# Kernel optimization log

Measured on AMD Instinct MI355X. Metric: run time of the kernel, lower is better.

The kernel has to match this reference:

```python
import jax, jax.numpy as jnp
import numpy as np

N = 50000   # nodes (= batch_size = num_e)
D = 256     # d_dim = n_hidden
E = 320000  # edges (first half 'in' direction, second half 'out'/inverse)
R = 400     # relation types (incl. inverses)


def setup_inputs() -> dict:
    key = jax.random.key(0)
    ks = jax.random.split(key, 12)
    s = 0.05  # weight scale so tanh stays in linear-ish range
    w = lambda k, shp: jax.random.normal(k, shp, jnp.float32) * s
    return {
        "emb": jax.random.normal(ks[0], (N, D), jnp.float32),
        "edge_index": jax.random.randint(ks[1], (2, E), 0, N),
        "edge_type": jax.random.randint(ks[2], (E,), 0, R),
        "rel1": w(ks[3], (R, D)),
        "W_in1": w(ks[4], (D, D)),
        "W_out1": w(ks[5], (D, D)),
        "W_loop1": w(ks[6], (D, D)),
        "b1": jnp.zeros((D,), jnp.float32),
        "rel2": w(ks[7], (R, D)),
        "W_in2": w(ks[8], (D, D)),
        "W_out2": w(ks[9], (D, D)),
        "W_loop2": w(ks[10], (D, D)),
        "b2": jnp.zeros((D,), jnp.float32),
        "res": jnp.array([0.1], jnp.float32),
        "mu_w": w(ks[11], (D, D)),
        "mu_b": jnp.zeros((D,), jnp.float32),
        "num_nodes": N,
    }


def _mgcn_conv(x, edge_index, edge_type, rel, W_in, W_out, W_loop, b, n):
    """Relational conv: gather -> compose with relation emb -> direction-split
    linear transform -> degree-normalized scatter-add -> self-loop -> tanh."""
    src, dst = edge_index[0], edge_index[1]
    e = edge_index.shape[1]
    half = e // 2
    m = x[src] * rel[edge_type]                                   # [E, D] compose ('mult')
    m = jnp.concatenate([m[:half] @ W_in, m[half:] @ W_out], 0)    # direction-specific transform
    deg = jax.ops.segment_sum(jnp.ones((e,), x.dtype), dst, num_segments=n)
    norm = 1.0 / jnp.maximum(deg, 1.0)                             # 1/in-degree
    agg = jax.ops.segment_sum(m * norm[dst][:, None], dst, num_segments=n)
    return jnp.tanh(agg + x @ W_loop + b)


def reference(emb, edge_index, edge_type,
              rel1, W_in1, W_out1, W_loop1, b1,
              rel2, W_in2, W_out2, W_loop2, b2,
              res, mu_w, mu_b, num_nodes):
    # forward_base with p.res=True, core_layer=2, dropout in eval mode (identity)
    h = emb + res * _mgcn_conv(emb, edge_index, edge_type, rel1, W_in1, W_out1, W_loop1, b1, num_nodes)
    h = h + res * _mgcn_conv(h, edge_index, edge_type, rel2, W_in2, W_out2, W_loop2, b2, num_nodes)
    # drift head f(t, y) = mu(forward_base(y))
    return h @ mu_w + mu_b
```

## Files before the change

### kernel.cpp

```cpp
#include <hip/hip_runtime.h>
#include <hip/hip_bf16.h>
#include <cstdint>
#include <cstddef>


typedef short bf16x8 __attribute__((ext_vector_type(8)));
typedef float f32x4  __attribute__((ext_vector_type(4)));

__device__ __forceinline__ float b2f(unsigned short u) {
    union { unsigned u32; float f; } c; c.u32 = ((unsigned)u) << 16; return c.f;
}
__device__ __forceinline__ unsigned short f2b(float f) {
    union { float f; unsigned u; } c; c.f = f;
    unsigned r = c.u + 0x7FFFu + ((c.u >> 16) & 1u);
    return (unsigned short)(r >> 16);
}
__device__ __forceinline__ float ftanh(float x) {
    float e = __expf(2.0f * x);
    return 1.0f - __fdividef(2.0f, e + 1.0f);
}


__global__ void k_hist(const int* __restrict__ dst, int* __restrict__ cnt, int E) {
    int i = blockIdx.x * blockDim.x + threadIdx.x;
    if (i < E) atomicAdd(&cnt[dst[i]], 1);
}

__global__ void k_norm(const int* __restrict__ cnt, float* __restrict__ norm, int N) {
    int i = blockIdx.x * blockDim.x + threadIdx.x;
    if (i < N) norm[i] = 1.0f / fmaxf((float)cnt[i], 1.0f);
}

__global__ void k_scan1(const int* __restrict__ cnt, int* __restrict__ part,
                        int* __restrict__ bsum, int N) {
    __shared__ int s[256];
    int i = blockIdx.x * 256 + threadIdx.x;
    int v = (i < N) ? cnt[i] : 0;
    s[threadIdx.x] = v; __syncthreads();
    #pragma unroll
    for (int o = 1; o < 256; o <<= 1) {
        int t = (threadIdx.x >= o) ? s[threadIdx.x - o] : 0;
        __syncthreads();
        s[threadIdx.x] += t;
        __syncthreads();
    }
    if (i < N) part[i] = s[threadIdx.x] - v;
    if (threadIdx.x == 255) bsum[blockIdx.x] = s[255];
}

__global__ void k_scan2(int* __restrict__ bsum, int nb) {
    __shared__ int s[256];
    int v = (threadIdx.x < nb) ? bsum[threadIdx.x] : 0;
    s[threadIdx.x] = v; __syncthreads();
    #pragma unroll
    for (int o = 1; o < 256; o <<= 1) {
        int t = (threadIdx.x >= o) ? s[threadIdx.x - o] : 0;
        __syncthreads();
        s[threadIdx.x] += t;
        __syncthreads();
    }
    if (threadIdx.x < nb) bsum[threadIdx.x] = s[threadIdx.x] - v;
}

__global__ void k_scan3(const int* __restrict__ part, const int* __restrict__ bsum,
                        int* __restrict__ rowptr, int* __restrict__ cursor, int N, int E) {
    int i = blockIdx.x * 256 + threadIdx.x;
    if (i < N) {
        int r = part[i] + bsum[blockIdx.x];
        rowptr[i] = r; cursor[i] = r;
    }
    if (i == 0) rowptr[N] = E;
}

__global__ void k_scatter(const int* __restrict__ src, const int* __restrict__ dst,
                          const int* __restrict__ et, int* __restrict__ cursor,
                          unsigned* __restrict__ erec, int E, int halfE) {
    int e = blockIdx.x * blockDim.x + threadIdx.x;
    if (e < E) {
        int d = dst[e];
        int pos = atomicAdd(&cursor[d], 1);
        unsigned rec = (unsigned)src[e] | ((unsigned)et[e] << 16)
                     | ((e >= halfE) ? 0x80000000u : 0u);
        erec[pos] = rec;
    }
}


__global__ void k_cvt3(const float* __restrict__ s0, unsigned short* __restrict__ d0, long n0,
                       const float* __restrict__ s1, unsigned short* __restrict__ d1, long n1,
                       const float* __restrict__ s2, unsigned short* __restrict__ d2, long n2) {
    long i = (long)blockIdx.x * blockDim.x + threadIdx.x;
    const float* s; unsigned short* d; long j = i;
    if (j < n0) { s = s0; d = d0; }
    else {
        j -= n0;
        if (j < n1) { s = s1; d = d1; }
        else { j -= n1; if (j >= n2) return; s = s2; d = d2; }
    }
    float4 v = ((const float4*)s)[j];
    ushort4 o;
    o.x = f2b(v.x); o.y = f2b(v.y); o.z = f2b(v.z); o.w = f2b(v.w);
    ((ushort4*)d)[j] = o;
}

__global__ void k_wfrag7(const float* __restrict__ w0, const float* __restrict__ w1,
                         const float* __restrict__ w2, const float* __restrict__ w3,
                         const float* __restrict__ w4, const float* __restrict__ w5,
                         const float* __restrict__ w6, unsigned short* __restrict__ out) {
    int o = blockIdx.x * 256 + threadIdx.x;
    int mi = o >> 16;
    int r  = o & 65535;
    const float* W = (mi == 0) ? w0 : (mi == 1) ? w1 : (mi == 2) ? w2 :
                     (mi == 3) ? w3 : (mi == 4) ? w4 : (mi == 5) ? w5 : w6;
    int j  = r & 7;
    int l  = (r >> 3) & 63;
    int nn = (r >> 9) & 15;
    int kg = r >> 13;
    int k = kg * 32 + (l >> 4) * 8 + j;
    int n = nn * 16 + (l & 15);
    out[o] = f2b(W[k * 256 + n]);
}


__global__ __launch_bounds__(256)
void k_agg(const unsigned short* __restrict__ xb, const unsigned short* __restrict__ relb,
           const int* __restrict__ rowptr, const unsigned* __restrict__ erec,
           const float* __restrict__ norm,
           unsigned short* __restrict__ sIn, unsigned short* __restrict__ sOut,
           int N, int D)
{
    const int w = threadIdx.x >> 6, l = threadIdx.x & 63;
    const int v = blockIdx.x * 4 + w;
    if (v >= N) return;
    const int rs = rowptr[v], re = rowptr[v + 1];
    const float nm = norm[v];

    float ai0 = 0, ai1 = 0, ai2 = 0, ai3 = 0;
    float ao0 = 0, ao1 = 0, ao2 = 0, ao3 = 0;

    unsigned c0 = (rs     < re) ? erec[rs]     : 0u;
    unsigned c1 = (rs + 1 < re) ? erec[rs + 1] : 0u;
    unsigned c2 = (rs + 2 < re) ? erec[rs + 2] : 0u;
    unsigned c3 = (rs + 3 < re) ? erec[rs + 3] : 0u;
    int i = rs;
    while (i + 4 <= re) {
        unsigned m0 = (i + 4 < re) ? erec[i + 4] : 0u;
        unsigned m1 = (i + 5 < re) ? erec[i + 5] : 0u;
        unsigned m2 = (i + 6 < re) ? erec[i + 6] : 0u;
        unsigned m3 = (i + 7 < re) ? erec[i + 7] : 0u;
        ushort4 x0 = *(const ushort4*)(xb   + (size_t)(c0 & 0xffff) * D + l * 4);
        ushort4 r0 = *(const ushort4*)(relb + (size_t)((c0 >> 16) & 0x7fff) * D + l * 4);
        ushort4 x1 = *(const ushort4*)(xb   + (size_t)(c1 & 0xffff) * D + l * 4);
        ushort4 r1 = *(const ushort4*)(relb + (size_t)((c1 >> 16) & 0x7fff) * D + l * 4);
        ushort4 x2 = *(const ushort4*)(xb   + (size_t)(c2 & 0xffff) * D + l * 4);
        ushort4 r2 = *(const ushort4*)(relb + (size_t)((c2 >> 16) & 0x7fff) * D + l * 4);
        ushort4 x3 = *(const ushort4*)(xb   + (size_t)(c3 & 0xffff) * D + l * 4);
        ushort4 r3 = *(const ushort4*)(relb + (size_t)((c3 >> 16) & 0x7fff) * D + l * 4);
        float p0, p1, p2, p3;
        p0 = b2f(x0.x)*b2f(r0.x); p1 = b2f(x0.y)*b2f(r0.y);
        p2 = b2f(x0.z)*b2f(r0.z); p3 = b2f(x0.w)*b2f(r0.w);
        if (c0 >> 31) { ao0 += p0; ao1 += p1; ao2 += p2; ao3 += p3; }
        else          { ai0 += p0; ai1 += p1; ai2 += p2; ai3 += p3; }
        p0 = b2f(x1.x)*b2f(r1.x); p1 = b2f(x1.y)*b2f(r1.y);
        p2 = b2f(x1.z)*b2f(r1.z); p3 = b2f(x1.w)*b2f(r1.w);
        if (c1 >> 31) { ao0 += p0; ao1 += p1; ao2 += p2; ao3 += p3; }
        else          { ai0 += p0; ai1 += p1; ai2 += p2; ai3 += p3; }
        p0 = b2f(x2.x)*b2f(r2.x); p1 = b2f(x2.y)*b2f(r2.y);
        p2 = b2f(x2.z)*b2f(r2.z); p3 = b2f(x2.w)*b2f(r2.w);
        if (c2 >> 31) { ao0 += p0; ao1 += p1; ao2 += p2; ao3 += p3; }
        else          { ai0 += p0; ai1 += p1; ai2 += p2; ai3 += p3; }
        p0 = b2f(x3.x)*b2f(r3.x); p1 = b2f(x3.y)*b2f(r3.y);
        p2 = b2f(x3.z)*b2f(r3.z); p3 = b2f(x3.w)*b2f(r3.w);
        if (c3 >> 31) { ao0 += p0; ao1 += p1; ao2 += p2; ao3 += p3; }
        else          { ai0 += p0; ai1 += p1; ai2 += p2; ai3 += p3; }
        c0 = m0; c1 = m1; c2 = m2; c3 = m3; i += 4;
    }
    #pragma unroll
    for (int j = 0; j < 3; ++j) {
        if (i + j < re) {
            unsigned cur = (j == 0) ? c0 : (j == 1) ? c1 : c2;
            ushort4 x0 = *(const ushort4*)(xb   + (size_t)(cur & 0xffff) * D + l * 4);
            ushort4 r0 = *(const ushort4*)(relb + (size_t)((cur >> 16) & 0x7fff) * D + l * 4);
            float p0 = b2f(x0.x)*b2f(r0.x), p1 = b2f(x0.y)*b2f(r0.y);
            float p2 = b2f(x0.z)*b2f(r0.z), p3 = b2f(x0.w)*b2f(r0.w);
            if (cur >> 31) { ao0 += p0; ao1 += p1; ao2 += p2; ao3 += p3; }
            else           { ai0 += p0; ai1 += p1; ai2 += p2; ai3 += p3; }
        }
    }

    ushort4 oi, oo;
    oi.x = f2b(ai0 * nm); oi.y = f2b(ai1 * nm); oi.z = f2b(ai2 * nm); oi.w = f2b(ai3 * nm);
    oo.x = f2b(ao0 * nm); oo.y = f2b(ao1 * nm); oo.z = f2b(ao2 * nm); oo.w = f2b(ao3 * nm);
    *(ushort4*)(sIn  + (size_t)v * D + l * 4) = oi;
    *(ushort4*)(sOut + (size_t)v * D + l * 4) = oo;
}


#define GIT(S, AtC, AtN, Rw0, Rw1, Rl0, Rl1)                                    \
  do {                                                                          \
    if ((S) + 1 < 12) {                                                         \
      *(uint4*)(&AtN[wo0]) = Rw0;                                               \
      *(uint4*)(&AtN[wo1]) = Rw1;                                               \
    }                                                                           \
    {                                                                           \
      const int p_ = (S) >> 2, cb_ = (S) & 3;                                   \
      const unsigned short* __restrict__ Wp_ = Wf + (size_t)p_ * 65536;         \
      _Pragma("unroll")                                                         \
      for (int kk_ = 0; kk_ < 2; ++kk_) {                                       \
        const int kg_ = cb_ * 2 + kk_;                                          \
        bf16x8 a_[4], b_[4];                                                    \
        _Pragma("unroll")                                                       \
        for (int m_ = 0; m_ < 4; ++m_) {                                        \
          int rm_ = 16 * m_ + lr;                                               \
          int ch_ = (kk_ * 4 + lq) ^ (rm_ & 7);                                 \
          a_[m_] = *(const bf16x8*)(&AtC[rm_ * 64 + ch_ * 8]);                  \
        }                                                                       \
        _Pragma("unroll")                                                       \
        for (int n_ = 0; n_ < 4; ++n_) {                                        \
          b_[n_] = *(const bf16x8*)(Wp_ + (((kg_ * 16 + (w * 4 + n_)) * 64 + l) * 8)); \
        }                                                                       \
        _Pragma("unroll")                                                       \
        for (int m_ = 0; m_ < 4; ++m_) {                                        \
          _Pragma("unroll")                                                     \
          for (int n_ = 0; n_ < 4; ++n_) {                                      \
            acc[m_][n_] = __builtin_amdgcn_mfma_f32_16x16x32_bf16(a_[m_], b_[n_], acc[m_][n_], 0, 0, 0); \
          }                                                                     \
        }                                                                       \
      }                                                                         \
    }                                                                           \
    if ((S) + 3 < 12) {                                                         \
      const int p3_ = ((S) + 3) >> 2, cb3_ = ((S) + 3) & 3;                     \
      const unsigned short* ap_ = (p3_ == 0) ? a0 : ((p3_ == 1) ? a1 : a2);     \
      Rl0 = *(const uint4*)(ap_ + g0 + cb3_ * 64);                              \
      Rl1 = *(const uint4*)(ap_ + g1 + cb3_ * 64);                              \
    }                                                                           \
    asm volatile("s_waitcnt lgkmcnt(0)" ::: "memory");                          \
    __builtin_amdgcn_sched_barrier(0);                                          \
    __builtin_amdgcn_s_barrier();                                               \
    __builtin_amdgcn_sched_barrier(0);                                          \
  } while (0)

template <bool HEAD>
__global__ __launch_bounds__(256, 4)
void k_gemm(const unsigned short* __restrict__ a0,
            const unsigned short* __restrict__ a1,
            const unsigned short* __restrict__ a2,
            const unsigned short* __restrict__ Wf,
            const float* __restrict__ bias,
            const float* __restrict__ resPtr,
            const unsigned short* __restrict__ WfMu,
            const float* __restrict__ mub,
            float* __restrict__ outF,
            unsigned short* __restrict__ outB,
            int N, int D)
{
    __shared__ unsigned short lds[HEAD ? 16384 : 8192];
    unsigned short* At0 = lds;
    unsigned short* At1 = lds + 4096;

    const int t = threadIdx.x;
    const int rBase = blockIdx.x * 64;

    const int w  = t >> 6;
    const int l  = t & 63;
    const int lr = l & 15;
    const int lq = l >> 4;

    const int rS0 = t >> 3;
    const int rS1 = rS0 + 32;
    const int cS  = t & 7;
    const int wo0 = rS0 * 64 + ((cS ^ (rS0 & 7)) * 8);
    const int wo1 = rS1 * 64 + ((cS ^ (rS1 & 7)) * 8);
    const size_t g0 = (size_t)min(rBase + rS0, N - 1) * D + cS * 8;
    const size_t g1 = (size_t)min(rBase + rS1, N - 1) * D + cS * 8;

    f32x4 acc[4][4] = {};
    uint4 Ra0, Ra1, Rb0, Rb1, Rc0, Rc1;

    Ra0 = *(const uint4*)(a0 + g0);
    Ra1 = *(const uint4*)(a0 + g1);
    Rb0 = *(const uint4*)(a0 + g0 + 64);
    Rb1 = *(const uint4*)(a0 + g1 + 64);
    Rc0 = *(const uint4*)(a0 + g0 + 128);
    Rc1 = *(const uint4*)(a0 + g1 + 128);
    *(uint4*)(&At0[wo0]) = Ra0;
    *(uint4*)(&At0[wo1]) = Ra1;
    asm volatile("s_waitcnt lgkmcnt(0)" ::: "memory");
    __builtin_amdgcn_sched_barrier(0);
    __builtin_amdgcn_s_barrier();
    __builtin_amdgcn_sched_barrier(0);

    GIT(0,  At0, At1, Rb0, Rb1, Ra0, Ra1);
    GIT(1,  At1, At0, Rc0, Rc1, Rb0, Rb1);
    GIT(2,  At0, At1, Ra0, Ra1, Rc0, Rc1);
    GIT(3,  At1, At0, Rb0, Rb1, Ra0, Ra1);
    GIT(4,  At0, At1, Rc0, Rc1, Rb0, Rb1);
    GIT(5,  At1, At0, Ra0, Ra1, Rc0, Rc1);
    GIT(6,  At0, At1, Rb0, Rb1, Ra0, Ra1);
    GIT(7,  At1, At0, Rc0, Rc1, Rb0, Rb1);
    GIT(8,  At0, At1, Ra0, Ra1, Rc0, Rc1);
    GIT(9,  At1, At0, Rb0, Rb1, Ra0, Ra1);
    GIT(10, At0, At1, Rc0, Rc1, Rb0, Rb1);
    GIT(11, At1, At0, Ra0, Ra1, Rc0, Rc1);

    const int rb4 = lq * 4;
    const float resv = resPtr[0];

    if (!HEAD) {
        unsigned short* C = lds;
        #pragma unroll
        for (int half = 0; half < 2; ++half) {
            if ((w >> 1) == half) {
                #pragma unroll
                for (int m = 0; m < 4; ++m) {
                    #pragma unroll
                    for (int i = 0; i < 4; ++i) {
                        int r6 = 16 * m + rb4 + i;
                        #pragma unroll
                        for (int n = 0; n < 4; ++n) {
                            int cH = (w & 1) * 64 + lr + 16 * n;
                            float v = acc[m][n][i] + bias[half * 128 + cH];
                            C[r6 * 128 + cH] = f2b(resv * ftanh(v));
                        }
                    }
                }
            }
            __syncthreads();
            #pragma unroll
            for (int ii = 0; ii < 4; ++ii) {
                int g   = ii * 256 + t;
                int r   = g >> 4;
                int cc  = g & 15;
                int row = rBase + r;
                if (row < N) {
                    bf16x8 sv = *(const bf16x8*)(&C[r * 128 + cc * 8]);
                    const unsigned short* ar = a0 + (size_t)row * D + half * 128 + cc * 8;
                    uint4 av = *(const uint4*)ar;
                    unsigned aw[4] = { av.x, av.y, av.z, av.w };
                    unsigned ow[4];
                    #pragma unroll
                    for (int p = 0; p < 4; ++p) {
                        float h0 = b2f((unsigned short)(aw[p] & 0xffff)) + b2f((unsigned short)sv[2 * p]);
                        float h1 = b2f((unsigned short)(aw[p] >> 16))    + b2f((unsigned short)sv[2 * p + 1]);
                        ow[p] = (unsigned)f2b(h0) | ((unsigned)f2b(h1) << 16);
                    }
                    *(uint4*)(outB + (size_t)row * D + half * 128 + cc * 8) =
                        make_uint4(ow[0], ow[1], ow[2], ow[3]);
                }
            }
            __syncthreads();
        }
    } else {
        #pragma unroll
        for (int m = 0; m < 4; ++m) {
            #pragma unroll
            for (int i = 0; i < 4; ++i) {
                int row = rBase + 16 * m + rb4 + i;
                if (row < N) {
                    size_t base = (size_t)row * D + w * 64 + lr;
                    int r6 = 16 * m + rb4 + i;
                    #pragma unroll
                    for (int n = 0; n < 4; ++n) {
                        int   c = w * 64 + lr + 16 * n;
                        float v = acc[m][n][i] + bias[c];
                        float h = b2f(a0[base + 16 * n]) + resv * ftanh(v);
                        lds[r6 * 256 + (c ^ ((r6 & 7) << 3))] = f2b(h);
                    }
                }
            }
        }
        __syncthreads();
        #pragma unroll
        for (int m = 0; m < 4; ++m) {
            #pragma unroll
            for (int n = 0; n < 4; ++n)
                acc[m][n] = (f32x4){0.f, 0.f, 0.f, 0.f};
        }

        #pragma unroll
        for (int s2 = 0; s2 < 4; ++s2) {
            #pragma unroll
            for (int kk = 0; kk < 2; ++kk) {
                const int kg = s2 * 2 + kk;
                bf16x8 a_[4], b_[4];
                #pragma unroll
                for (int m = 0; m < 4; ++m) {
                    int rm = 16 * m + lr;
                    int ch = (s2 * 8 + kk * 4 + lq) ^ (rm & 7);
                    a_[m] = *(const bf16x8*)(&lds[rm * 256 + ch * 8]);
                }
                #pragma unroll
                for (int n = 0; n < 4; ++n)
                    b_[n] = *(const bf16x8*)(WfMu + (((kg * 16 + (w * 4 + n)) * 64 + l) * 8));
                #pragma unroll
                for (int m = 0; m < 4; ++m) {
                    #pragma unroll
                    for (int n = 0; n < 4; ++n)
                        acc[m][n] = __builtin_amdgcn_mfma_f32_16x16x32_bf16(a_[m], b_[n], acc[m][n], 0, 0, 0);
                }
            }
        }

        __syncthreads();
        float* Cf = (float*)lds;
        #pragma unroll
        for (int half = 0; half < 2; ++half) {
            if ((w >> 1) == half) {
                #pragma unroll
                for (int m = 0; m < 4; ++m) {
                    #pragma unroll
                    for (int i = 0; i < 4; ++i) {
                        int r6 = 16 * m + rb4 + i;
                        #pragma unroll
                        for (int n = 0; n < 4; ++n) {
                            int cH = (w & 1) * 64 + lr + 16 * n;
                            Cf[r6 * 128 + cH] = acc[m][n][i] + mub[half * 128 + cH];
                        }
                    }
                }
            }
            __syncthreads();
            #pragma unroll
            for (int ii = 0; ii < 8; ++ii) {
                int g   = ii * 256 + t;
                int r   = g >> 5;
                int cc  = g & 31;
                int row = rBase + r;
                if (row < N) {
                    *(float4*)(outF + (size_t)row * D + half * 128 + cc * 4) =
                        *(const float4*)(&Cf[r * 128 + cc * 4]);
                }
            }
            __syncthreads();
        }
    }
}


extern "C" void kernel_launch(void* const* d_in, const int* in_sizes, int n_in,
                              void* d_out, int out_size, void* d_ws, size_t ws_size,
                              hipStream_t stream)
{
    const float* emb  = (const float*)d_in[0];
    const int*   ei   = (const int*)  d_in[1];
    const int*   et   = (const int*)  d_in[2];
    const float* rel1 = (const float*)d_in[3];
    const float* Wi1  = (const float*)d_in[4];
    const float* Wo1  = (const float*)d_in[5];
    const float* Wl1  = (const float*)d_in[6];
    const float* b1   = (const float*)d_in[7];
    const float* rel2 = (const float*)d_in[8];
    const float* Wi2  = (const float*)d_in[9];
    const float* Wo2  = (const float*)d_in[10];
    const float* Wl2  = (const float*)d_in[11];
    const float* b2   = (const float*)d_in[12];
    const float* res  = (const float*)d_in[13];
    const float* muw  = (const float*)d_in[14];
    const float* mub  = (const float*)d_in[15];

    const int D = in_sizes[7];
    const int N = in_sizes[0] / D;
    const int E = in_sizes[2];
    const int R = in_sizes[3] / D;
    const int halfE = E / 2;
    const int* srcA = ei;
    const int* dstA = ei + E;
    const size_t DD = (size_t)D * D;

    char* ws = (char*)d_ws;
    size_t off = 0;
    auto alloc = [&](size_t bytes) -> char* {
        char* p = ws + off; off += (bytes + 255) & ~(size_t)255; return p;
    };
    const int nb1 = (N + 255) / 256;

    float*          norm   = (float*)          alloc((size_t)N * 4);
    int*            cnt    = (int*)            alloc((size_t)N * 4);
    int*            rowptr = (int*)            alloc((size_t)(N + 1) * 4);
    int*            cursor = (int*)            alloc((size_t)N * 4);
    int*            part   = (int*)            alloc((size_t)N * 4);
    int*            bsum   = (int*)            alloc(1024);
    unsigned*       erec   = (unsigned*)       alloc((size_t)E * 4);
    unsigned short* xb     = (unsigned short*) alloc((size_t)N * D * 2);
    unsigned short* h1b    = (unsigned short*) alloc((size_t)N * D * 2);
    unsigned short* sIn    = (unsigned short*) alloc((size_t)N * D * 2);
    unsigned short* sOut   = (unsigned short*) alloc((size_t)N * D * 2);
    unsigned short* r1b    = (unsigned short*) alloc((size_t)R * D * 2);
    unsigned short* r2b    = (unsigned short*) alloc((size_t)R * D * 2);
    unsigned short* fAll   = (unsigned short*) alloc(7 * DD * 2);
    if (off > ws_size) return;

    unsigned short* fW1 = fAll;
    unsigned short* fW2 = fAll + 3 * DD;
    unsigned short* fMu = fAll + 6 * DD;

    hipMemsetAsync(cnt, 0, (size_t)N * 4, stream);
    k_hist   <<<(E + 255) / 256, 256, 0, stream>>>(dstA, cnt, E);
    k_norm   <<<nb1, 256, 0, stream>>>(cnt, norm, N);
    k_scan1  <<<nb1, 256, 0, stream>>>(cnt, part, bsum, N);
    k_scan2  <<<1,   256, 0, stream>>>(bsum, nb1);
    k_scan3  <<<nb1, 256, 0, stream>>>(part, bsum, rowptr, cursor, N, E);
    k_scatter<<<(E + 255) / 256, 256, 0, stream>>>(srcA, dstA, et, cursor, erec, E, halfE);

    long nd4 = (long)N * D / 4, rd4 = (long)R * D / 4;
    long tot4 = nd4 + 2 * rd4;
    k_cvt3<<<(int)((tot4 + 255) / 256), 256, 0, stream>>>(
        emb, xb, nd4, rel1, r1b, rd4, rel2, r2b, rd4);
    k_wfrag7<<<(int)(7 * DD / 256), 256, 0, stream>>>(
        Wl1, Wi1, Wo1, Wl2, Wi2, Wo2, muw, fAll);

    const int AB = (N + 3) / 4;
    const int NB = (N + 63) / 64;

    k_agg<<<AB, 256, 0, stream>>>(xb, r1b, rowptr, erec, norm, sIn, sOut, N, D);
    k_gemm<false><<<NB, 256, 0, stream>>>(xb, sIn, sOut, fW1, b1, res,
                                          nullptr, nullptr, nullptr, h1b, N, D);

    k_agg<<<AB, 256, 0, stream>>>(h1b, r2b, rowptr, erec, norm, sIn, sOut, N, D);
    k_gemm<true><<<NB, 256, 0, stream>>>(h1b, sIn, sOut, fW2, b2, res,
                                         fMu, mub, (float*)d_out, nullptr, N, D);
}
```

Baseline: 240.7 us.

## Double-buffer weight fragments in registers to prefetch next k-step

The GEMM main loop now loads the next stage's weight (B) fragments from global memory into a second register buffer while the current stage's MFMAs run from the first, instead of loading B right before use. This is meant to hide global-load latency for the weights. Launch bounds drop from 4 to 2 blocks per SM so the extra 16 vector registers fit, which lowers potential occupancy.

```diff
diff --git a/kernel.cpp b/kernel.cpp
--- a/kernel.cpp
+++ b/kernel.cpp
@@ -196,19 +196,30 @@
 }
 
 
-#define GIT(S, AtC, AtN, Rw0, Rw1, Rl0, Rl1)                                    \
+#define GIT(S, AtC, AtN, Rw0, Rw1, Rl0, Rl1, Bc, Bn)                            \
   do {                                                                          \
     if ((S) + 1 < 12) {                                                         \
       *(uint4*)(&AtN[wo0]) = Rw0;                                               \
       *(uint4*)(&AtN[wo1]) = Rw1;                                               \
     }                                                                           \
-    {                                                                           \
-      const int p_ = (S) >> 2, cb_ = (S) & 3;                                   \
-      const unsigned short* __restrict__ Wp_ = Wf + (size_t)p_ * 65536;         \
+    if ((S) + 1 < 12) {                                                         \
+      const int pn_ = ((S) + 1) >> 2, cbn_ = ((S) + 1) & 3;                     \
+      const unsigned short* __restrict__ Wn_ = Wf + (size_t)pn_ * 65536;        \
       _Pragma("unroll")                                                         \
       for (int kk_ = 0; kk_ < 2; ++kk_) {                                       \
-        const int kg_ = cb_ * 2 + kk_;                                          \
-        bf16x8 a_[4], b_[4];                                                    \
+        _Pragma("unroll")                                                       \
+        for (int n_ = 0; n_ < 4; ++n_) {                                        \
+          Bn[kk_ * 4 + n_] = *(const bf16x8*)(Wn_ +                             \
+              ((((cbn_ * 2 + kk_) * 16 + (w * 4 + n_)) * 64 + l) * 8));         \
+        }                                                                       \
+      }                                                                         \
+    }                                                                           \
+    {                                                                           \
+      const int cb_ = (S) & 3;                                                  \
+      _Pragma("unroll")                                                         \
+      for (int kk_ = 0; kk_ < 2; ++kk_) {                                       \
+        (void)cb_;                                                              \
+        bf16x8 a_[4];                                                           \
         _Pragma("unroll")                                                       \
         for (int m_ = 0; m_ < 4; ++m_) {                                        \
           int rm_ = 16 * m_ + lr;                                               \
@@ -216,14 +227,10 @@
           a_[m_] = *(const bf16x8*)(&AtC[rm_ * 64 + ch_ * 8]);                  \
         }                                                                       \
         _Pragma("unroll")                                                       \
-        for (int n_ = 0; n_ < 4; ++n_) {                                        \
-          b_[n_] = *(const bf16x8*)(Wp_ + (((kg_ * 16 + (w * 4 + n_)) * 64 + l) * 8)); \
-        }                                                                       \
-        _Pragma("unroll")                                                       \
         for (int m_ = 0; m_ < 4; ++m_) {                                        \
           _Pragma("unroll")                                                     \
           for (int n_ = 0; n_ < 4; ++n_) {                                      \
-            acc[m_][n_] = __builtin_amdgcn_mfma_f32_16x16x32_bf16(a_[m_], b_[n_], acc[m_][n_], 0, 0, 0); \
+            acc[m_][n_] = __builtin_amdgcn_mfma_f32_16x16x32_bf16(a_[m_], Bc[kk_ * 4 + n_], acc[m_][n_], 0, 0, 0); \
           }                                                                     \
         }                                                                       \
       }                                                                         \
@@ -241,7 +248,7 @@
   } while (0)
 
 template <bool HEAD>
-__global__ __launch_bounds__(256, 4)
+__global__ __launch_bounds__(256, 2)
 void k_gemm(const unsigned short* __restrict__ a0,
             const unsigned short* __restrict__ a1,
             const unsigned short* __restrict__ a2,
@@ -276,6 +283,7 @@
 
     f32x4 acc[4][4] = {};
     uint4 Ra0, Ra1, Rb0, Rb1, Rc0, Rc1;
+    bf16x8 B0[8], B1[8];
 
     Ra0 = *(const uint4*)(a0 + g0);
     Ra1 = *(const uint4*)(a0 + g1);
@@ -283,6 +291,12 @@
     Rb1 = *(const uint4*)(a0 + g1 + 64);
     Rc0 = *(const uint4*)(a0 + g0 + 128);
     Rc1 = *(const uint4*)(a0 + g1 + 128);
+    #pragma unroll
+    for (int kk = 0; kk < 2; ++kk) {
+        #pragma unroll
+        for (int n = 0; n < 4; ++n)
+            B0[kk * 4 + n] = *(const bf16x8*)(Wf + (((kk * 16 + (w * 4 + n)) * 64 + l) * 8));
+    }
     *(uint4*)(&At0[wo0]) = Ra0;
     *(uint4*)(&At0[wo1]) = Ra1;
     asm volatile("s_waitcnt lgkmcnt(0)" ::: "memory");
@@ -290,18 +304,18 @@
     __builtin_amdgcn_s_barrier();
     __builtin_amdgcn_sched_barrier(0);
 
-    GIT(0,  At0, At1, Rb0, Rb1, Ra0, Ra1);
-    GIT(1,  At1, At0, Rc0, Rc1, Rb0, Rb1);
-    GIT(2,  At0, At1, Ra0, Ra1, Rc0, Rc1);
-    GIT(3,  At1, At0, Rb0, Rb1, Ra0, Ra1);
-    GIT(4,  At0, At1, Rc0, Rc1, Rb0, Rb1);
-    GIT(5,  At1, At0, Ra0, Ra1, Rc0, Rc1);
-    GIT(6,  At0, At1, Rb0, Rb1, Ra0, Ra1);
-    GIT(7,  At1, At0, Rc0, Rc1, Rb0, Rb1);
-    GIT(8,  At0, At1, Ra0, Ra1, Rc0, Rc1);
-    GIT(9,  At1, At0, Rb0, Rb1, Ra0, Ra1);
-    GIT(10, At0, At1, Rc0, Rc1, Rb0, Rb1);
-    GIT(11, At1, At0, Ra0, Ra1, Rc0, Rc1);
+    GIT(0,  At0, At1, Rb0, Rb1, Ra0, Ra1, B0, B1);
+    GIT(1,  At1, At0, Rc0, Rc1, Rb0, Rb1, B1, B0);
+    GIT(2,  At0, At1, Ra0, Ra1, Rc0, Rc1, B0, B1);
+    GIT(3,  At1, At0, Rb0, Rb1, Ra0, Ra1, B1, B0);
+    GIT(4,  At0, At1, Rc0, Rc1, Rb0, Rb1, B0, B1);
+    GIT(5,  At1, At0, Ra0, Ra1, Rc0, Rc1, B1, B0);
+    GIT(6,  At0, At1, Rb0, Rb1, Ra0, Ra1, B0, B1);
+    GIT(7,  At1, At0, Rc0, Rc1, Rb0, Rb1, B1, B0);
+    GIT(8,  At0, At1, Ra0, Ra1, Rc0, Rc1, B0, B1);
+    GIT(9,  At1, At0, Rb0, Rb1, Ra0, Ra1, B1, B0);
+    GIT(10, At0, At1, Rc0, Rc1, Rb0, Rb1, B0, B1);
+    GIT(11, At1, At0, Ra0, Ra1, Rc0, Rc1, B1, B0);
 
     const int rb4 = lq * 4;
     const float resv = resPtr[0];
```

Result: faster. 229.1 us (-4.8%).

## Load GEMM A operands directly from global memory, dropping LDS staging pipeline

Applied to the files above, without the earlier changes.

Replaces the register-prefetched, double-buffered LDS staging of the A tile (with a barrier per k-step) with direct per-lane global loads of A fragments feeding MFMA, all three input parts walked in one unrolled loop. This removes the LDS writes, the LDS reads and the twelve block barriers, but each wave now loads its own A rows from global/L2 with no software prefetch, so latency is hidden only by occupancy and the compiler's scheduling. Launch bounds drop to 3 blocks per SM to allow more registers, and the epilogue barrier is moved so the trailing sync is skipped.

```diff
diff --git a/kernel.cpp b/kernel.cpp
--- a/kernel.cpp
+++ b/kernel.cpp
@@ -196,52 +196,8 @@
 }
 
 
-#define GIT(S, AtC, AtN, Rw0, Rw1, Rl0, Rl1)                                    \
-  do {                                                                          \
-    if ((S) + 1 < 12) {                                                         \
-      *(uint4*)(&AtN[wo0]) = Rw0;                                               \
-      *(uint4*)(&AtN[wo1]) = Rw1;                                               \
-    }                                                                           \
-    {                                                                           \
-      const int p_ = (S) >> 2, cb_ = (S) & 3;                                   \
-      const unsigned short* __restrict__ Wp_ = Wf + (size_t)p_ * 65536;         \
-      _Pragma("unroll")                                                         \
-      for (int kk_ = 0; kk_ < 2; ++kk_) {                                       \
-        const int kg_ = cb_ * 2 + kk_;                                          \
-        bf16x8 a_[4], b_[4];                                                    \
-        _Pragma("unroll")                                                       \
-        for (int m_ = 0; m_ < 4; ++m_) {                                        \
-          int rm_ = 16 * m_ + lr;                                               \
-          int ch_ = (kk_ * 4 + lq) ^ (rm_ & 7);                                 \
-          a_[m_] = *(const bf16x8*)(&AtC[rm_ * 64 + ch_ * 8]);                  \
-        }                                                                       \
-        _Pragma("unroll")                                                       \
-        for (int n_ = 0; n_ < 4; ++n_) {                                        \
-          b_[n_] = *(const bf16x8*)(Wp_ + (((kg_ * 16 + (w * 4 + n_)) * 64 + l) * 8)); \
-        }                                                                       \
-        _Pragma("unroll")                                                       \
-        for (int m_ = 0; m_ < 4; ++m_) {                                        \
-          _Pragma("unroll")                                                     \
-          for (int n_ = 0; n_ < 4; ++n_) {                                      \
-            acc[m_][n_] = __builtin_amdgcn_mfma_f32_16x16x32_bf16(a_[m_], b_[n_], acc[m_][n_], 0, 0, 0); \
-          }                                                                     \
-        }                                                                       \
-      }                                                                         \
-    }                                                                           \
-    if ((S) + 3 < 12) {                                                         \
-      const int p3_ = ((S) + 3) >> 2, cb3_ = ((S) + 3) & 3;                     \
-      const unsigned short* ap_ = (p3_ == 0) ? a0 : ((p3_ == 1) ? a1 : a2);     \
-      Rl0 = *(const uint4*)(ap_ + g0 + cb3_ * 64);                              \
-      Rl1 = *(const uint4*)(ap_ + g1 + cb3_ * 64);                              \
-    }                                                                           \
-    asm volatile("s_waitcnt lgkmcnt(0)" ::: "memory");                          \
-    __builtin_amdgcn_sched_barrier(0);                                          \
-    __builtin_amdgcn_s_barrier();                                               \
-    __builtin_amdgcn_sched_barrier(0);                                          \
-  } while (0)
-
 template <bool HEAD>
-__global__ __launch_bounds__(256, 4)
+__global__ __launch_bounds__(256, 3)
 void k_gemm(const unsigned short* __restrict__ a0,
             const unsigned short* __restrict__ a1,
             const unsigned short* __restrict__ a2,
@@ -255,8 +211,6 @@
             int N, int D)
 {
     __shared__ unsigned short lds[HEAD ? 16384 : 8192];
-    unsigned short* At0 = lds;
-    unsigned short* At1 = lds + 4096;
 
     const int t = threadIdx.x;
     const int rBase = blockIdx.x * 64;
@@ -266,42 +220,36 @@
     const int lr = l & 15;
     const int lq = l >> 4;
 
-    const int rS0 = t >> 3;
-    const int rS1 = rS0 + 32;
-    const int cS  = t & 7;
-    const int wo0 = rS0 * 64 + ((cS ^ (rS0 & 7)) * 8);
-    const int wo1 = rS1 * 64 + ((cS ^ (rS1 & 7)) * 8);
-    const size_t g0 = (size_t)min(rBase + rS0, N - 1) * D + cS * 8;
-    const size_t g1 = (size_t)min(rBase + rS1, N - 1) * D + cS * 8;
+    const unsigned short* arow0;
+    int rA[4];
+    #pragma unroll
+    for (int m = 0; m < 4; ++m)
+        rA[m] = min(rBase + 16 * m + lr, N - 1);
+    (void)arow0;
 
     f32x4 acc[4][4] = {};
-    uint4 Ra0, Ra1, Rb0, Rb1, Rc0, Rc1;
-
-    Ra0 = *(const uint4*)(a0 + g0);
-    Ra1 = *(const uint4*)(a0 + g1);
-    Rb0 = *(const uint4*)(a0 + g0 + 64);
-    Rb1 = *(const uint4*)(a0 + g1 + 64);
-    Rc0 = *(const uint4*)(a0 + g0 + 128);
-    Rc1 = *(const uint4*)(a0 + g1 + 128);
-    *(uint4*)(&At0[wo0]) = Ra0;
-    *(uint4*)(&At0[wo1]) = Ra1;
-    asm volatile("s_waitcnt lgkmcnt(0)" ::: "memory");
-    __builtin_amdgcn_sched_barrier(0);
-    __builtin_amdgcn_s_barrier();
-    __builtin_amdgcn_sched_barrier(0);
-
-    GIT(0,  At0, At1, Rb0, Rb1, Ra0, Ra1);
-    GIT(1,  At1, At0, Rc0, Rc1, Rb0, Rb1);
-    GIT(2,  At0, At1, Ra0, Ra1, Rc0, Rc1);
-    GIT(3,  At1, At0, Rb0, Rb1, Ra0, Ra1);
-    GIT(4,  At0, At1, Rc0, Rc1, Rb0, Rb1);
-    GIT(5,  At1, At0, Ra0, Ra1, Rc0, Rc1);
-    GIT(6,  At0, At1, Rb0, Rb1, Ra0, Ra1);
-    GIT(7,  At1, At0, Rc0, Rc1, Rb0, Rb1);
-    GIT(8,  At0, At1, Ra0, Ra1, Rc0, Rc1);
-    GIT(9,  At1, At0, Rb0, Rb1, Ra0, Ra1);
-    GIT(10, At0, At1, Rc0, Rc1, Rb0, Rb1);
-    GIT(11, At1, At0, Ra0, Ra1, Rc0, Rc1);
+
+    #pragma unroll
+    for (int p = 0; p < 3; ++p) {
+        const unsigned short* __restrict__ ap = (p == 0) ? a0 : ((p == 1) ? a1 : a2);
+        const unsigned short* __restrict__ Wp = Wf + (size_t)p * 65536;
+        #pragma unroll
+        for (int kq = 0; kq < 8; ++kq) {
+            bf16x8 a_[4], b_[4];
+            #pragma unroll
+            for (int m = 0; m < 4; ++m)
+                a_[m] = *(const bf16x8*)(ap + (size_t)rA[m] * 256 + kq * 32 + lq * 8);
+            #pragma unroll
+            for (int n = 0; n < 4; ++n)
+                b_[n] = *(const bf16x8*)(Wp + (((kq * 16 + (w * 4 + n)) * 64 + l) * 8));
+            #pragma unroll
+            for (int m = 0; m < 4; ++m) {
+                #pragma unroll
+                for (int n = 0; n < 4; ++n)
+                    acc[m][n] = __builtin_amdgcn_mfma_f32_16x16x32_bf16(a_[m], b_[n], acc[m][n], 0, 0, 0);
+            }
+        }
+    }
 
     const int rb4 = lq * 4;
     const float resv = resPtr[0];
@@ -310,6 +258,7 @@
         unsigned short* C = lds;
         #pragma unroll
         for (int half = 0; half < 2; ++half) {
+            if (half) __syncthreads();
             if ((w >> 1) == half) {
                 #pragma unroll
                 for (int m = 0; m < 4; ++m) {
@@ -348,7 +297,6 @@
                         make_uint4(ow[0], ow[1], ow[2], ow[3]);
                 }
             }
-            __syncthreads();
         }
     } else {
         #pragma unroll
```

Result: slower. 313.6 us (+30.3%).
